# Kernel tuning notes

Hardware: AMD Instinct MI355X
Metric: run time of the kernel (lower is better)

Reference implementation:

```python
import jax, jax.numpy as jnp
import numpy as np

EPS = 1e-5
NUM_GROUPS = 32


def group_norm(x, scale, bias):
    # x: [B, C, H, W], 32 groups, normalized over (C/G, H, W)
    B, C, H, W = x.shape
    G = NUM_GROUPS
    xg = x.reshape(B, G, C // G, H, W)
    mean = xg.mean(axis=(2, 3, 4), keepdims=True)
    var = xg.var(axis=(2, 3, 4), keepdims=True)
    xg = (xg - mean) * jax.lax.rsqrt(var + EPS)
    x = xg.reshape(B, C, H, W)
    return x * scale[None, :, None, None] + bias[None, :, None, None]


def setup_inputs() -> dict:
    key = jax.random.key(0)
    ks = jax.random.split(key, 6)
    B, C, H, W = 32, 512, 32, 32
    std = 1.0 / np.sqrt(C)
    return {
        "x": jax.random.normal(ks[0], (B, C, H, W), dtype=jnp.float32),
        "gn_scale": jnp.ones((C,), dtype=jnp.float32),
        "gn_bias": jnp.zeros((C,), dtype=jnp.float32),
        "wq": jax.random.normal(ks[1], (C, C), dtype=jnp.float32) * std,
        "bq": jnp.zeros((C,), dtype=jnp.float32),
        "wk": jax.random.normal(ks[2], (C, C), dtype=jnp.float32) * std,
        "bk": jnp.zeros((C,), dtype=jnp.float32),
        "wv": jax.random.normal(ks[3], (C, C), dtype=jnp.float32) * std,
        "bv": jnp.zeros((C,), dtype=jnp.float32),
        "wo": jax.random.normal(ks[4], (C, C), dtype=jnp.float32) * std,
        "bo": jnp.zeros((C,), dtype=jnp.float32),
    }


def reference(x, gn_scale, gn_bias, wq, bq, wk, bk, wv, bv, wo, bo):
    B, C, H, W = x.shape
    h = group_norm(x, gn_scale, gn_bias)
    # 1x1 convs == per-pixel matmuls; flatten spatial to tokens: [B, HW, C]
    ht = h.reshape(B, C, H * W).transpose(0, 2, 1)
    q = jnp.einsum('bnc,oc->bno', ht, wq) + bq  # [B, HW, C]
    k = jnp.einsum('bnc,oc->bno', ht, wk) + bk
    v = jnp.einsum('bnc,oc->bno', ht, wv) + bv
    scale = 1.0 / jnp.sqrt(jnp.asarray(C, x.dtype))
    w = jnp.einsum('bnc,bmc->bnm', q, k) * scale  # [B, HW, HW]
    w = jax.nn.softmax(w, axis=-1)
    a = jnp.einsum('bnm,bmc->bnc', w, v)  # [B, HW, C]
    out = jnp.einsum('bnc,oc->bno', a, wo) + bo
    out = out.transpose(0, 2, 1).reshape(B, C, H, W)
    return x + out
```

## Files before the change

### kernel.cpp

```cpp
#include <hip/hip_runtime.h>
#include <hip/hip_bf16.h>
#include <stdint.h>

typedef unsigned short u16;
typedef __attribute__((ext_vector_type(8))) short short8;
typedef __attribute__((ext_vector_type(4))) short s16x4;
typedef __attribute__((ext_vector_type(4))) float f32x4;

#define NTOK 1024
#define CDIM 512
#define NG 32

#define GLOAD_LDS16(gptr, lptr)                                                              \
  __builtin_amdgcn_global_load_lds((const __attribute__((address_space(1))) unsigned int*)(gptr), \
                                   (__attribute__((address_space(3))) unsigned int*)(lptr), 16, 0, 0)

__device__ __forceinline__ u16 f2bf(float f) {
  __hip_bfloat16 h = __float2bfloat16(f);
  union { __hip_bfloat16 h; u16 u; } v; v.h = h;
  return v.u;
}

__device__ __forceinline__ float bf2f(u16 b) {
  union { uint32_t u; float f; } v; v.u = ((uint32_t)b) << 16;
  return v.f;
}

__global__ __launch_bounds__(256) void prep_stats(const float* __restrict__ x,
                                                  const float* __restrict__ wq, const float* __restrict__ wk,
                                                  const float* __restrict__ wv, const float* __restrict__ wo,
                                                  const float* __restrict__ bq, const float* __restrict__ bk,
                                                  const float* __restrict__ bv,
                                                  u16* __restrict__ wout, float* __restrict__ bqkv,
                                                  float* __restrict__ rsum,
                                                  float* __restrict__ mean_o, float* __restrict__ rstd_o) {
  int bg = blockIdx.x;
  int i = bg * 256 + threadIdx.x;
  wout[i]          = f2bf(wq[i]);
  wout[262144 + i] = f2bf(wk[i]);
  wout[524288 + i] = f2bf(wv[i]);
  wout[786432 + i] = f2bf(wo[i]);
  if (i < 512) bqkv[i] = bq[i];
  else if (i < 1024) bqkv[i] = bk[i - 512];
  else if (i < 1536) bqkv[i] = bv[i - 1024];
  if (i < 32768) rsum[i] = 0.f;

  const float4* base = (const float4*)(x + (size_t)bg * 16384);
  float s = 0.f, ss = 0.f;
  for (int k = threadIdx.x; k < 4096; k += 256) {
    float4 v = base[k];
    s  += v.x + v.y + v.z + v.w;
    ss += v.x * v.x + v.y * v.y + v.z * v.z + v.w * v.w;
  }
#pragma unroll
  for (int d = 1; d < 64; d <<= 1) { s += __shfl_xor(s, d); ss += __shfl_xor(ss, d); }
  __shared__ float as[4], as2[4];
  int w = threadIdx.x >> 6;
  if ((threadIdx.x & 63) == 0) { as[w] = s; as2[w] = ss; }
  __syncthreads();
  if (threadIdx.x == 0) {
    float S = as[0] + as[1] + as[2] + as[3];
    float SS = as2[0] + as2[1] + as2[2] + as2[3];
    float m = S * (1.f / 16384.f);
    float var = SS * (1.f / 16384.f) - m * m;
    mean_o[bg] = m;
    rstd_o[bg] = rsqrtf(var + 1e-5f);
  }
}

__global__ __launch_bounds__(256) void gn_apply(const float* __restrict__ x,
                                                const float* __restrict__ mean_, const float* __restrict__ rstd_,
                                                const float* __restrict__ gsc, const float* __restrict__ gbi,
                                                u16* __restrict__ h) {
  int n0 = blockIdx.x * 64, c0 = blockIdx.y * 64, b = blockIdx.z;
  __shared__ u16 t[64][65];
  int tid = threadIdx.x;
  int nl4 = (tid & 15) * 4;
  int clb = tid >> 4;
#pragma unroll
  for (int p = 0; p < 4; ++p) {
    int cl = p * 16 + clb;
    int c = c0 + cl;
    int g = c >> 4;
    float m = mean_[b * NG + g], rs = rstd_[b * NG + g];
    float sc = gsc[c] * rs, bi = gbi[c] - m * sc;
    float4 v = *(const float4*)(x + ((size_t)b * CDIM + c) * NTOK + n0 + nl4);
    t[cl][nl4 + 0] = f2bf(v.x * sc + bi);
    t[cl][nl4 + 1] = f2bf(v.y * sc + bi);
    t[cl][nl4 + 2] = f2bf(v.z * sc + bi);
    t[cl][nl4 + 3] = f2bf(v.w * sc + bi);
  }
  __syncthreads();
  int nl = tid >> 3;
  int cc = (tid & 7) * 8;
#pragma unroll
  for (int p = 0; p < 2; ++p) {
    int n = nl + p * 32;
    short8 o;
#pragma unroll
    for (int i = 0; i < 8; ++i) o[i] = (short)t[cc + i][n];
    *(short8*)(h + (size_t)(b * NTOK + n0 + n) * CDIM + c0 + cc) = o;
  }
}

template <int MODE>
__device__ __forceinline__ void gemm_body(const u16* __restrict__ A, const u16* __restrict__ B,
                                          const float* __restrict__ bias, u16* __restrict__ outb,
                                          u16* __restrict__ outb2,
                                          float* __restrict__ outf, const float* __restrict__ resid,
                                          int Ka, int Kb, int nkt,
                                          size_t strideA, size_t strideB, int batch0) {
  int nx = gridDim.x, ny = gridDim.y;
  int nwg = nx * ny * gridDim.z;
  int id = blockIdx.x + nx * (blockIdx.y + ny * blockIdx.z);
  int cpx = nwg >> 3;
  int sw = (id & 7) * cpx + (id >> 3);
  int bx = sw % nx; int t_ = sw / nx;
  int by = t_ % ny; int z = t_ / ny;

  const u16* Amat = A + (size_t)z * strideA;
  const u16* Bmat = B + (size_t)z * strideB;
  int n0 = bx * 256, m0 = by * 256;
  __shared__ __align__(16) u16 SH[65536];
  int tid = threadIdx.x;
  int l = tid & 63, wid = tid >> 6;
  int lr = l & 15, lh = l >> 4;
  int wm = (wid >> 2) * 128;
  int wn = (wid & 3) * 64;

  f32x4 acc[8][4];
#pragma unroll
  for (int i = 0; i < 8; ++i)
#pragma unroll
    for (int j = 0; j < 4; ++j) acc[i][j] = (f32x4){0.f, 0.f, 0.f, 0.f};

  short8 af[4][2];
  short8 bf01[2][2];
  short8 bf23[2][2];

  int sr = tid >> 3, sc = tid & 7;
  int sg = (sc ^ (sr & 7)) << 3;
  const u16* Ag0 = Amat + (size_t)(m0 + sr) * Ka + sg;
  const u16* Ag1 = Ag0 + (size_t)64 * Ka;
  const u16* Bg0 = Bmat + (size_t)(n0 + sr) * Kb + sg;
  const u16* Bg1 = Bg0 + (size_t)64 * Kb;
  size_t hA = (size_t)128 * Ka, hB = (size_t)128 * Kb;
  u16* Al0 = SH + sr * 64 + sc * 8;
  u16* Bl0 = SH + 32768 + sr * 64 + sc * 8;

#define STAGE_A(bufsel, ktv, half)                                        \
  {                                                                       \
    size_t go_ = (size_t)(ktv) * 64 + ((half) ? hA : (size_t)0);          \
    u16* ld_ = Al0 + (bufsel) * 16384 + (half) * 8192;                    \
    GLOAD_LDS16(Ag0 + go_, ld_);                                          \
    GLOAD_LDS16(Ag1 + go_, ld_ + 4096);                                   \
  }
#define STAGE_B(bufsel, ktv, half)                                        \
  {                                                                       \
    size_t go_ = (size_t)(ktv) * 64 + ((half) ? hB : (size_t)0);          \
    u16* ld_ = Bl0 + (bufsel) * 16384 + (half) * 8192;                    \
    GLOAD_LDS16(Bg0 + go_, ld_);                                          \
    GLOAD_LDS16(Bg1 + go_, ld_ + 4096);                                   \
  }

#define READ_AF(ihalf, bufsel)                                                        \
  _Pragma("unroll") for (int i_ = 0; i_ < 4; ++i_) {                                  \
    int row_ = wm + (ihalf) * 64 + i_ * 16 + lr;                                      \
    const u16* p_ = SH + (bufsel) * 16384 + row_ * 64;                                \
    _Pragma("unroll") for (int ks_ = 0; ks_ < 2; ++ks_)                               \
      af[i_][ks_] = *(const short8*)(p_ + (((ks_ * 4 + lh) ^ (row_ & 7)) << 3));      \
  }

#define READ_BF(dst, jbase, bufsel)                                                   \
  _Pragma("unroll") for (int j_ = 0; j_ < 2; ++j_) {                                  \
    int row_ = wn + ((jbase) + j_) * 16 + lr;                                         \
    const u16* p_ = SH + 32768 + (bufsel) * 16384 + row_ * 64;                        \
    _Pragma("unroll") for (int ks_ = 0; ks_ < 2; ++ks_)                               \
      dst[j_][ks_] = *(const short8*)(p_ + (((ks_ * 4 + lh) ^ (row_ & 7)) << 3));     \
  }

#define MFMA_Q(ihalf, jbase, bsrc)                                                    \
  _Pragma("unroll") for (int ks_ = 0; ks_ < 2; ++ks_)                                 \
    _Pragma("unroll") for (int i_ = 0; i_ < 4; ++i_)                                  \
      _Pragma("unroll") for (int j_ = 0; j_ < 2; ++j_)                                \
        acc[(ihalf) * 4 + i_][(jbase) + j_] = __builtin_amdgcn_mfma_f32_16x16x32_bf16( \
            af[i_][ks_], bsrc[j_][ks_], acc[(ihalf) * 4 + i_][(jbase) + j_], 0, 0, 0);

#define PBAR() __builtin_amdgcn_s_barrier()

#define PHASES(BC, BN, GI, DOHI, DOLO)                                    \
  {                                                                       \
    int g1_ = (GI) + 1, g2_ = (GI) + 2;                                   \
                                           \
    READ_AF(0, BC);                                                       \
    READ_BF(bf01, 0, BC);                                                 \
    if (DOHI) { STAGE_A(BN, g1_, 1); }                                    \
    PBAR();                                                               \
    __builtin_amdgcn_s_setprio(1);                                        \
    MFMA_Q(0, 0, bf01);                                                   \
    __builtin_amdgcn_s_setprio(0);                                        \
    PBAR();                                                               \
                                           \
    READ_BF(bf23, 2, BC);                                                 \
    if (DOHI) { STAGE_B(BN, g1_, 1); }                                    \
    PBAR();                                                               \
    __builtin_amdgcn_s_setprio(1);                                        \
    MFMA_Q(0, 2, bf23);                                                   \
    __builtin_amdgcn_s_setprio(0);                                        \
    PBAR();                                                               \
     \
    READ_AF(1, BC);                                                       \
    if (DOLO) { STAGE_B(BC, g2_, 0); }                                    \
    PBAR();                                                               \
    __builtin_amdgcn_s_setprio(1);                                        \
    MFMA_Q(1, 2, bf23);                                                   \
    __builtin_amdgcn_s_setprio(0);                                        \
    PBAR();                                                               \
     \
    if (DOLO) { STAGE_A(BC, g2_, 0); }                                    \
    PBAR();                                                               \
    __builtin_amdgcn_s_setprio(1);                                        \
    MFMA_Q(1, 0, bf01);                                                   \
    __builtin_amdgcn_s_setprio(0);                                        \
    if (DOLO) { asm volatile("s_waitcnt vmcnt(4)"); }                     \
    else      { asm volatile("s_waitcnt vmcnt(0)"); }                     \
    __builtin_amdgcn_sched_barrier(0);                                    \
    PBAR();                                                               \
  }

  int k1 = (1 < nkt) ? 1 : 0;
  STAGE_B(0, 0, 0);
  STAGE_A(0, 0, 0);
  STAGE_A(0, 0, 1);
  STAGE_B(0, 0, 1);
  STAGE_B(1, k1, 0);
  STAGE_A(1, k1, 0);
  asm volatile("s_waitcnt vmcnt(4)");
  __builtin_amdgcn_sched_barrier(0);
  PBAR();

  for (int kt = 0; kt < nkt; kt += 2) {
    int more = (kt + 2 < nkt) ? 1 : 0;
    PHASES(0, 1, kt, 1, more);
    PHASES(1, 0, kt + 1, more, more);
  }

  __syncthreads();
  const int gr0 = m0 + wm, gc0 = n0 + wn;
  u16* eb = SH + wid * 4352;

  if constexpr (MODE == 5) {
    float bj[4];
#pragma unroll
    for (int j = 0; j < 4; ++j) bj[j] = bias[gc0 + j * 16 + lr];
    if (n0 < 1024) {
#pragma unroll
      for (int pass = 0; pass < 2; ++pass) {
#pragma unroll
        for (int i2 = 0; i2 < 4; ++i2)
#pragma unroll
          for (int j = 0; j < 4; ++j)
#pragma unroll
            for (int r = 0; r < 4; ++r)
              eb[(i2 * 16 + lh * 4 + r) * 68 + j * 16 + lr] =
                  f2bf(acc[pass * 4 + i2][j][r] + bj[j]);
        asm volatile("s_waitcnt lgkmcnt(0)");
        __builtin_amdgcn_sched_barrier(0);
#pragma unroll
        for (int t = 0; t < 8; ++t) {
          int row = t * 8 + (l >> 3), c8 = (l & 7) * 8;
          s16x4 lo = *(const s16x4*)(eb + row * 68 + c8);
          s16x4 hi = *(const s16x4*)(eb + row * 68 + c8 + 4);
          short8 o;
          o[0] = lo[0]; o[1] = lo[1]; o[2] = lo[2]; o[3] = lo[3];
          o[4] = hi[0]; o[5] = hi[1]; o[6] = hi[2]; o[7] = hi[3];
          *(short8*)(outb + (size_t)(gr0 + pass * 64 + row) * 1024 + gc0 + c8) = o;
        }
        asm volatile("s_waitcnt lgkmcnt(0)");
        __builtin_amdgcn_sched_barrier(0);
      }
    } else {
      int ch0 = gc0 - 1024;
      int bt = m0 >> 10, tok0 = (m0 & 1023) + wm;
#pragma unroll
      for (int pass = 0; pass < 2; ++pass) {
#pragma unroll
        for (int i2 = 0; i2 < 4; ++i2)
#pragma unroll
          for (int j = 0; j < 4; ++j) {
            s16x4 w;
#pragma unroll
            for (int r = 0; r < 4; ++r)
              w[r] = (short)f2bf(acc[pass * 4 + i2][j][r] + bj[j]);
            *(s16x4*)(eb + (j * 16 + lr) * 68 + i2 * 16 + lh * 4) = w;
          }
        asm volatile("s_waitcnt lgkmcnt(0)");
        __builtin_amdgcn_sched_barrier(0);
#pragma unroll
        for (int t = 0; t < 8; ++t) {
          int row = t * 8 + (l >> 3), c8 = (l & 7) * 8;
          s16x4 lo = *(const s16x4*)(eb + row * 68 + c8);
          s16x4 hi = *(const s16x4*)(eb + row * 68 + c8 + 4);
          short8 o;
          o[0] = lo[0]; o[1] = lo[1]; o[2] = lo[2]; o[3] = lo[3];
          o[4] = hi[0]; o[5] = hi[1]; o[6] = hi[2]; o[7] = hi[3];
          *(short8*)(outb2 + (size_t)(bt * 512 + ch0 + row) * 1024 + tok0 + pass * 64 + c8) = o;
        }
        asm volatile("s_waitcnt lgkmcnt(0)");
        __builtin_amdgcn_sched_barrier(0);
      }
    }
  } else if constexpr (MODE == 3) {
    const float k2 = 0.063758716f;
    u16* obase = outb + (size_t)z * 1048576;
    float* rsb = outf + (size_t)z * 1024;
#pragma unroll
    for (int pass = 0; pass < 2; ++pass) {
#pragma unroll
      for (int i2 = 0; i2 < 4; ++i2)
#pragma unroll
        for (int r = 0; r < 4; ++r) {
          float rp = 0.f;
#pragma unroll
          for (int j = 0; j < 4; ++j) {
            float e = exp2f(acc[pass * 4 + i2][j][r] * k2);
            rp += e;
            eb[(i2 * 16 + lh * 4 + r) * 68 + j * 16 + lr] = f2bf(e);
          }
          rp += __shfl_xor(rp, 1);
          rp += __shfl_xor(rp, 2);
          rp += __shfl_xor(rp, 4);
          rp += __shfl_xor(rp, 8);
          if (lr == 0) atomicAdd(rsb + gr0 + pass * 64 + i2 * 16 + lh * 4 + r, rp);
        }
      asm volatile("s_waitcnt lgkmcnt(0)");
      __builtin_amdgcn_sched_barrier(0);
#pragma unroll
      for (int t = 0; t < 8; ++t) {
        int row = t * 8 + (l >> 3), c8 = (l & 7) * 8;
        s16x4 lo = *(const s16x4*)(eb + row * 68 + c8);
        s16x4 hi = *(const s16x4*)(eb + row * 68 + c8 + 4);
        short8 o;
        o[0] = lo[0]; o[1] = lo[1]; o[2] = lo[2]; o[3] = lo[3];
        o[4] = hi[0]; o[5] = hi[1]; o[6] = hi[2]; o[7] = hi[3];
        *(short8*)(obase + (size_t)(gr0 + pass * 64 + row) * 1024 + gc0 + c8) = o;
      }
      asm volatile("s_waitcnt lgkmcnt(0)");
      __builtin_amdgcn_sched_barrier(0);
    }
  } else if constexpr (MODE == 4) {
    const float* rsg = outf + (size_t)z * 1024;
    u16* obase = outb + (size_t)(batch0 + z) * 524288;
#pragma unroll
    for (int pass = 0; pass < 2; ++pass) {
#pragma unroll
      for (int i2 = 0; i2 < 4; ++i2)
#pragma unroll
        for (int r = 0; r < 4; ++r) {
          float inv_ = 1.f / rsg[gr0 + pass * 64 + i2 * 16 + lh * 4 + r];
#pragma unroll
          for (int j = 0; j < 4; ++j)
            eb[(i2 * 16 + lh * 4 + r) * 68 + j * 16 + lr] =
                f2bf(acc[pass * 4 + i2][j][r] * inv_);
        }
      asm volatile("s_waitcnt lgkmcnt(0)");
      __builtin_amdgcn_sched_barrier(0);
#pragma unroll
      for (int t = 0; t < 8; ++t) {
        int row = t * 8 + (l >> 3), c8 = (l & 7) * 8;
        s16x4 lo = *(const s16x4*)(eb + row * 68 + c8);
        s16x4 hi = *(const s16x4*)(eb + row * 68 + c8 + 4);
        short8 o;
        o[0] = lo[0]; o[1] = lo[1]; o[2] = lo[2]; o[3] = lo[3];
        o[4] = hi[0]; o[5] = hi[1]; o[6] = hi[2]; o[7] = hi[3];
        *(short8*)(obase + (size_t)(gr0 + pass * 64 + row) * 512 + gc0 + c8) = o;
      }
      asm volatile("s_waitcnt lgkmcnt(0)");
      __builtin_amdgcn_sched_barrier(0);
    }
  } else {
    float* ebf = (float*)SH + wid * 2176;
    int bt = n0 >> 10, nn0 = (n0 & 1023) + wn;
#pragma unroll
    for (int pass = 0; pass < 4; ++pass) {
#pragma unroll
      for (int i2 = 0; i2 < 2; ++i2)
#pragma unroll
        for (int r = 0; r < 4; ++r) {
          float bv = bias[gr0 + pass * 32 + i2 * 16 + lh * 4 + r];
#pragma unroll
          for (int j = 0; j < 4; ++j)
            ebf[(i2 * 16 + lh * 4 + r) * 68 + j * 16 + lr] =
                acc[pass * 2 + i2][j][r] + bv;
        }
      asm volatile("s_waitcnt lgkmcnt(0)");
      __builtin_amdgcn_sched_barrier(0);
#pragma unroll
      for (int t = 0; t < 8; ++t) {
        int row = t * 4 + (l >> 4), c4 = (l & 15) * 4;
        float4 vv = *(const float4*)(ebf + row * 68 + c4);
        size_t addr = ((size_t)bt * 512 + gr0 + pass * 32 + row) * 1024 + nn0 + c4;
        const float4 rr = *(const float4*)(resid + addr);
        vv.x += rr.x; vv.y += rr.y; vv.z += rr.z; vv.w += rr.w;
        *(float4*)(outf + addr) = vv;
      }
      asm volatile("s_waitcnt lgkmcnt(0)");
      __builtin_amdgcn_sched_barrier(0);
    }
  }
#undef STAGE_A
#undef STAGE_B
#undef READ_AF
#undef READ_BF
#undef MFMA_Q
#undef PBAR
#undef PHASES
}

__global__ __launch_bounds__(512, 2) void gemm_qkv(const u16* A, const u16* B, const float* bias,
                                                   u16* outb, u16* outb2, float* outf, const float* resid,
                                                   int Ka, int Kb, int nkt, size_t sA, size_t sB, int b0) {
  gemm_body<5>(A, B, bias, outb, outb2, outf, resid, Ka, Kb, nkt, sA, sB, b0);
}
__global__ __launch_bounds__(512, 2) void gemm_o(const u16* A, const u16* B, const float* bias,
                                                 u16* outb, u16* outb2, float* outf, const float* resid,
                                                 int Ka, int Kb, int nkt, size_t sA, size_t sB, int b0) {
  gemm_body<2>(A, B, bias, outb, outb2, outf, resid, Ka, Kb, nkt, sA, sB, b0);
}
__global__ __launch_bounds__(512, 2) void gemm_s(const u16* A, const u16* B, const float* bias,
                                                 u16* outb, u16* outb2, float* outf, const float* resid,
                                                 int Ka, int Kb, int nkt, size_t sA, size_t sB, int b0) {
  gemm_body<3>(A, B, bias, outb, outb2, outf, resid, Ka, Kb, nkt, sA, sB, b0);
}
__global__ __launch_bounds__(512, 2) void gemm_pv(const u16* A, const u16* B, const float* bias,
                                                  u16* outb, u16* outb2, float* outf, const float* resid,
                                                  int Ka, int Kb, int nkt, size_t sA, size_t sB, int b0) {
  gemm_body<4>(A, B, bias, outb, outb2, outf, resid, Ka, Kb, nkt, sA, sB, b0);
}

extern "C" void kernel_launch(void* const* d_in, const int* in_sizes, int n_in,
                              void* d_out, int out_size, void* d_ws, size_t ws_size,
                              hipStream_t stream) {
  const float* x   = (const float*)d_in[0];
  const float* gsc = (const float*)d_in[1];
  const float* gbi = (const float*)d_in[2];
  const float* wq  = (const float*)d_in[3];
  const float* bq  = (const float*)d_in[4];
  const float* wk  = (const float*)d_in[5];
  const float* bk  = (const float*)d_in[6];
  const float* wv  = (const float*)d_in[7];
  const float* bv  = (const float*)d_in[8];
  const float* wo  = (const float*)d_in[9];
  const float* bo  = (const float*)d_in[10];

  char* ws = (char*)d_ws;
  u16* wbf = (u16*)ws;
  float* bqkv = (float*)(ws + (2ull << 20));
  float* mean_ = (float*)(ws + (2ull << 20) + 65536);
  float* rstd_ = mean_ + 1024;
  float* rsum = (float*)(ws + (3ull << 20));
  u16* h   = (u16*)(ws + (4ull << 20));
  u16* qk  = (u16*)(ws + (36ull << 20));
  u16* vm  = (u16*)(ws + (100ull << 20));
  u16* S   = (u16*)(ws + (132ull << 20));
  u16* am  = h;
  float* out = (float*)d_out;

  size_t sbytes = ws_size > (132ull << 20) ? ws_size - (132ull << 20) : 0;
  int CB = 1;
  while (CB < 32 && (size_t)(CB * 2) * (2ull << 20) <= sbytes) CB *= 2;

  prep_stats<<<1024, 256, 0, stream>>>(x, wq, wk, wv, wo, bq, bk, bv, wbf, bqkv, rsum, mean_, rstd_);
  gn_apply<<<dim3(16, 8, 32), 256, 0, stream>>>(x, mean_, rstd_, gsc, gbi, h);
  gemm_qkv<<<dim3(6, 128), 512, 0, stream>>>(h, wbf, bqkv, qk, vm, nullptr, nullptr,
                                             512, 512, 8, 0, 0, 0);
  for (int c0 = 0; c0 < 32; c0 += CB) {
    gemm_s<<<dim3(4, 4, CB), 512, 0, stream>>>(qk + (size_t)c0 * 1048576, qk + 512 + (size_t)c0 * 1048576,
                                               nullptr, S, nullptr, rsum + (size_t)c0 * 1024, nullptr,
                                               1024, 1024, 8, 1048576, 1048576, 0);
    gemm_pv<<<dim3(2, 4, CB), 512, 0, stream>>>(S, vm + (size_t)c0 * 524288,
                                                nullptr, am, nullptr, rsum + (size_t)c0 * 1024, nullptr,
                                                1024, 1024, 16, 1048576, 524288, c0);
  }
  gemm_o<<<dim3(128, 2), 512, 0, stream>>>(wbf + 786432, am, bo, nullptr, nullptr, out, x,
                                           512, 512, 8, 0, 0, 0);
}
```

Before: 225.3 us.

## Give output projection its own 256-thread GEMM with smaller tiles and triple buffering

Moves the output-projection GEMM out of the shared templated body into a dedicated kernel. It uses 256-thread blocks with 256x128 tiles and a K-step of 32, staged through a three-buffer global-to-LDS pipeline with swizzled rows. The grid doubles to 512 blocks to improve occupancy and load balance across CUs. The cost is fewer MFMAs per barrier and more blocks re-reading the weight tiles.

```diff
diff --git a/kernel.cpp b/kernel.cpp
--- a/kernel.cpp
+++ b/kernel.cpp
@@ -378,35 +378,6 @@
       asm volatile("s_waitcnt lgkmcnt(0)");
       __builtin_amdgcn_sched_barrier(0);
     }
-  } else {
-    float* ebf = (float*)SH + wid * 2176;
-    int bt = n0 >> 10, nn0 = (n0 & 1023) + wn;
-#pragma unroll
-    for (int pass = 0; pass < 4; ++pass) {
-#pragma unroll
-      for (int i2 = 0; i2 < 2; ++i2)
-#pragma unroll
-        for (int r = 0; r < 4; ++r) {
-          float bv = bias[gr0 + pass * 32 + i2 * 16 + lh * 4 + r];
-#pragma unroll
-          for (int j = 0; j < 4; ++j)
-            ebf[(i2 * 16 + lh * 4 + r) * 68 + j * 16 + lr] =
-                acc[pass * 2 + i2][j][r] + bv;
-        }
-      asm volatile("s_waitcnt lgkmcnt(0)");
-      __builtin_amdgcn_sched_barrier(0);
-#pragma unroll
-      for (int t = 0; t < 8; ++t) {
-        int row = t * 4 + (l >> 4), c4 = (l & 15) * 4;
-        float4 vv = *(const float4*)(ebf + row * 68 + c4);
-        size_t addr = ((size_t)bt * 512 + gr0 + pass * 32 + row) * 1024 + nn0 + c4;
-        const float4 rr = *(const float4*)(resid + addr);
-        vv.x += rr.x; vv.y += rr.y; vv.z += rr.z; vv.w += rr.w;
-        *(float4*)(outf + addr) = vv;
-      }
-      asm volatile("s_waitcnt lgkmcnt(0)");
-      __builtin_amdgcn_sched_barrier(0);
-    }
   }
 #undef STAGE_A
 #undef STAGE_B
@@ -417,15 +388,129 @@
 #undef PHASES
 }
 
+__device__ __forceinline__ void gemm_body_o(const u16* __restrict__ A, const u16* __restrict__ B,
+                                            const float* __restrict__ bias,
+                                            float* __restrict__ outf, const float* __restrict__ resid,
+                                            int Ka, int Kb, int nkt) {
+  int nx = gridDim.x, ny = gridDim.y;
+  int nwg = nx * ny;
+  int id = blockIdx.x + nx * blockIdx.y;
+  int cpx = nwg >> 3;
+  int sw = (id & 7) * cpx + (id >> 3);
+  int bx = sw % nx; int by = sw / nx;
+
+  int n0 = bx * 128, m0 = by * 256;
+  __shared__ __align__(16) u16 SH[36864];
+  int tid = threadIdx.x;
+  int l = tid & 63, wid = tid >> 6;
+  int lr = l & 15, lh = l >> 4;
+  int wm = (wid >> 1) * 128;
+  int wn = (wid & 1) * 64;
+
+  f32x4 acc[8][4];
+#pragma unroll
+  for (int i = 0; i < 8; ++i)
+#pragma unroll
+    for (int j = 0; j < 4; ++j) acc[i][j] = (f32x4){0.f, 0.f, 0.f, 0.f};
+
+  short8 af[8];
+  short8 bfr[4];
+
+  int sr = tid >> 2, sc4 = tid & 3;
+  int sg = (sc4 ^ ((sr >> 1) & 3)) * 8;
+  const u16* Ag0 = A + (size_t)(m0 + sr) * Ka + sg;
+  const u16* Bg0 = B + (size_t)(n0 + sr) * Kb + sg;
+  u16* Al0 = SH + sr * 32 + sc4 * 8;
+  u16* Bl0 = SH + 24576 + sr * 32 + sc4 * 8;
+
+  int rch = (lh ^ ((lr >> 1) & 3)) * 8;
+
+#define STG(bufsel, ktv)                                                          \
+  {                                                                               \
+    GLOAD_LDS16(Ag0 + (ktv) * 32,                       Al0 + (bufsel) * 8192);   \
+    GLOAD_LDS16(Ag0 + (ktv) * 32 + (size_t)64  * Ka,    Al0 + (bufsel) * 8192 + 2048); \
+    GLOAD_LDS16(Ag0 + (ktv) * 32 + (size_t)128 * Ka,    Al0 + (bufsel) * 8192 + 4096); \
+    GLOAD_LDS16(Ag0 + (ktv) * 32 + (size_t)192 * Ka,    Al0 + (bufsel) * 8192 + 6144); \
+    GLOAD_LDS16(Bg0 + (ktv) * 32,                       Bl0 + (bufsel) * 4096);   \
+    GLOAD_LDS16(Bg0 + (ktv) * 32 + (size_t)64  * Kb,    Bl0 + (bufsel) * 4096 + 2048); \
+  }
+
+#define RDF(bufsel)                                                                   \
+  _Pragma("unroll") for (int i_ = 0; i_ < 8; ++i_)                                    \
+    af[i_] = *(const short8*)(SH + (bufsel) * 8192 + (wm + i_ * 16 + lr) * 32 + rch); \
+  _Pragma("unroll") for (int j_ = 0; j_ < 4; ++j_)                                    \
+    bfr[j_] = *(const short8*)(SH + 24576 + (bufsel) * 4096 + (wn + j_ * 16 + lr) * 32 + rch);
+
+#define MFM32()                                                                       \
+  _Pragma("unroll") for (int i_ = 0; i_ < 8; ++i_)                                    \
+    _Pragma("unroll") for (int j_ = 0; j_ < 4; ++j_)                                  \
+      acc[i_][j_] = __builtin_amdgcn_mfma_f32_16x16x32_bf16(af[i_], bfr[j_], acc[i_][j_], 0, 0, 0);
+
+  STG(0, 0);
+  STG(1, 1);
+  asm volatile("s_waitcnt vmcnt(6)");
+  __builtin_amdgcn_sched_barrier(0);
+  __builtin_amdgcn_s_barrier();
+
+  int bc = 0, bs = 2;
+  for (int t = 0; t < nkt; ++t) {
+    const bool more = (t + 2 < nkt);
+    if (more) STG(bs, t + 2);
+    RDF(bc);
+    __builtin_amdgcn_s_setprio(1);
+    MFM32();
+    __builtin_amdgcn_s_setprio(0);
+    if (more) { asm volatile("s_waitcnt vmcnt(6)"); }
+    else      { asm volatile("s_waitcnt vmcnt(0)"); }
+    __builtin_amdgcn_sched_barrier(0);
+    __builtin_amdgcn_s_barrier();
+    bc = (bc == 2) ? 0 : bc + 1;
+    bs = (bs == 2) ? 0 : bs + 1;
+  }
+
+  __syncthreads();
+  const int gr0 = m0 + wm, gc0 = n0 + wn;
+  float* ebf = (float*)SH + wid * 2176;
+  int bt = n0 >> 10, nn0 = (n0 & 1023) + wn;
+#pragma unroll
+  for (int pass = 0; pass < 4; ++pass) {
+#pragma unroll
+    for (int i2 = 0; i2 < 2; ++i2)
+#pragma unroll
+      for (int r = 0; r < 4; ++r) {
+        float bv = bias[gr0 + pass * 32 + i2 * 16 + lh * 4 + r];
+#pragma unroll
+        for (int j = 0; j < 4; ++j)
+          ebf[(i2 * 16 + lh * 4 + r) * 68 + j * 16 + lr] = acc[pass * 2 + i2][j][r] + bv;
+      }
+    asm volatile("s_waitcnt lgkmcnt(0)");
+    __builtin_amdgcn_sched_barrier(0);
+#pragma unroll
+    for (int t = 0; t < 8; ++t) {
+      int row = t * 4 + (l >> 4), c4 = (l & 15) * 4;
+      float4 vv = *(const float4*)(ebf + row * 68 + c4);
+      size_t addr = ((size_t)bt * 512 + gr0 + pass * 32 + row) * 1024 + nn0 + c4;
+      const float4 rr = *(const float4*)(resid + addr);
+      vv.x += rr.x; vv.y += rr.y; vv.z += rr.z; vv.w += rr.w;
+      *(float4*)(outf + addr) = vv;
+    }
+    asm volatile("s_waitcnt lgkmcnt(0)");
+    __builtin_amdgcn_sched_barrier(0);
+  }
+#undef STG
+#undef RDF
+#undef MFM32
+}
+
 __global__ __launch_bounds__(512, 2) void gemm_qkv(const u16* A, const u16* B, const float* bias,
                                                    u16* outb, u16* outb2, float* outf, const float* resid,
                                                    int Ka, int Kb, int nkt, size_t sA, size_t sB, int b0) {
   gemm_body<5>(A, B, bias, outb, outb2, outf, resid, Ka, Kb, nkt, sA, sB, b0);
 }
-__global__ __launch_bounds__(512, 2) void gemm_o(const u16* A, const u16* B, const float* bias,
-                                                 u16* outb, u16* outb2, float* outf, const float* resid,
-                                                 int Ka, int Kb, int nkt, size_t sA, size_t sB, int b0) {
-  gemm_body<2>(A, B, bias, outb, outb2, outf, resid, Ka, Kb, nkt, sA, sB, b0);
+__global__ __launch_bounds__(256, 2) void gemm_o(const u16* A, const u16* B, const float* bias,
+                                                 float* outf, const float* resid,
+                                                 int Ka, int Kb, int nkt) {
+  gemm_body_o(A, B, bias, outf, resid, Ka, Kb, nkt);
 }
 __global__ __launch_bounds__(512, 2) void gemm_s(const u16* A, const u16* B, const float* bias,
                                                  u16* outb, u16* outb2, float* outf, const float* resid,
@@ -482,6 +567,5 @@
                                                 nullptr, am, nullptr, rsum + (size_t)c0 * 1024, nullptr,
                                                 1024, 1024, 16, 1048576, 524288, c0);
   }
-  gemm_o<<<dim3(128, 2), 512, 0, stream>>>(wbf + 786432, am, bo, nullptr, nullptr, out, x,
-                                           512, 512, 8, 0, 0, 0);
-}
+  gemm_o<<<dim3(256, 2), 256, 0, stream>>>(wbf + 786432, am, bo, out, x, 512, 512, 16);
+}
```

After: 225.1 us. Within noise of the previous version (-0.1%).
